# Optimization experiments

Measured on AMD Instinct MI355X. Metric: run time of the kernel, lower is better.

The kernel has to match this reference:

```python
import jax, jax.numpy as jnp
import numpy as np

B, S, HID = 4, 2048, 512
NH, HD = 8, 64
MAX_REL = 512


def setup_inputs() -> dict:
    key = jax.random.key(0)
    ks = jax.random.split(key, 10)
    sd = 0.02
    return {
        "hidden_states": jax.random.normal(ks[0], (B, S, HID), jnp.float32),
        "attention_mask": jnp.ones((B, S), jnp.float32),
        "Wq": jax.random.normal(ks[1], (HID, HID), jnp.float32) * sd,
        "bq": jnp.zeros((HID,), jnp.float32),
        "Wk": jax.random.normal(ks[2], (HID, HID), jnp.float32) * sd,
        "bk": jnp.zeros((HID,), jnp.float32),
        "Wv": jax.random.normal(ks[3], (HID, HID), jnp.float32) * sd,
        "bv": jnp.zeros((HID,), jnp.float32),
        "Wo": jax.random.normal(ks[4], (HID, HID), jnp.float32) * sd,
        "bo": jnp.zeros((HID,), jnp.float32),
        "rel_table": jax.random.normal(ks[5], (2 * MAX_REL + 1, NH), jnp.float32) * sd,
    }


def _heads(x):
    # [B,S,HID] -> [B,NH,S,HD]
    return x.reshape(B, S, NH, HD).transpose(0, 2, 1, 3)


def reference(hidden_states, attention_mask, Wq, bq, Wk, bk, Wv, bv, Wo, bo, rel_table):
    q = _heads(hidden_states @ Wq + bq)
    k = _heads(hidden_states @ Wk + bk)
    v = _heads(hidden_states @ Wv + bv)

    scores = jnp.einsum("bhqd,bhkd->bhqk", q, k) / jnp.sqrt(jnp.float32(HD))

    # relative position bias: rel[i,j] = clip(j-i, -MAX_REL, MAX_REL) + MAX_REL
    pos = jnp.arange(S)
    rel = jnp.clip(pos[None, :] - pos[:, None], -MAX_REL, MAX_REL) + MAX_REL
    bias = rel_table[rel]                      # [S,S,NH]
    bias = bias.transpose(2, 0, 1)             # [NH,S,S]
    scores = scores + bias[None]

    # mask: 1 attend, 0 masked
    neg = jnp.finfo(scores.dtype).min
    scores = scores + (1.0 - attention_mask)[:, None, None, :] * neg

    probs = jax.nn.softmax(scores, axis=-1)
    ctx = jnp.einsum("bhqk,bhkd->bhqd", probs, v)
    ctx = ctx.transpose(0, 2, 1, 3).reshape(B, S, HID)
    return ctx @ Wo + bo
```

## Files before the change

kernel.cpp:

```cpp
#include <hip/hip_runtime.h>
#include <hip/hip_bf16.h>

#define B_    4
#define S_    2048
#define HID_  512
#define NH_   8
#define HD_   64
#define MAXREL 512
#define M_    (B_ * S_)

#define LOG2E 1.44269504f
#define SCALE_Q (0.125f * LOG2E)

typedef __attribute__((ext_vector_type(8))) short bf8;
typedef __attribute__((ext_vector_type(4))) float f4;
typedef __attribute__((ext_vector_type(16))) float f16f;

static __device__ __forceinline__ unsigned short f2bf(float f) {
    union { float f; unsigned int u; } v; v.f = f;
    unsigned int u = v.u;
    unsigned int r = (u + 0x7FFFu + ((u >> 16) & 1u)) >> 16;
    return (unsigned short)r;
}

static __device__ __forceinline__ float ex2(float x) {
    float r; asm("v_exp_f32 %0, %1" : "=v"(r) : "v"(x)); return r;
}

static __device__ __forceinline__ void gload16(const void* g, void* l) {
    __builtin_amdgcn_global_load_lds(
        (const __attribute__((address_space(1))) unsigned int*)g,
        (__attribute__((address_space(3))) unsigned int*)l, 16, 0, 0);
}

#define MFMA16(a, b, c) __builtin_amdgcn_mfma_f32_16x16x32_bf16((a), (b), (c), 0, 0, 0)
#define MFMA32(a, b, c) __builtin_amdgcn_mfma_f32_32x32x16_bf16((a), (b), (c), 0, 0, 0)

__global__ void k_cast_hs(const float* __restrict__ src, unsigned short* __restrict__ dst, int n4) {
    int i = blockIdx.x * blockDim.x + threadIdx.x;
    if (i >= n4) return;
    float4 v = ((const float4*)src)[i];
    ushort4 o;
    o.x = f2bf(v.x); o.y = f2bf(v.y); o.z = f2bf(v.z); o.w = f2bf(v.w);
    ((ushort4*)dst)[i] = o;
}

__global__ void k_prep_mask(const float* __restrict__ mask, float* __restrict__ maskadd) {
    int i = blockIdx.x * blockDim.x + threadIdx.x;
    if (i < M_) maskadd[i] = (1.0f - mask[i]) * -3.0e38f;
}

__global__ void k_transpose_w4(const float* __restrict__ W0, const float* __restrict__ W1,
                               const float* __restrict__ W2, const float* __restrict__ W3,
                               unsigned short* __restrict__ T0, unsigned short* __restrict__ T1,
                               unsigned short* __restrict__ T2, unsigned short* __restrict__ T3) {
    __shared__ float tile[32][33];
    const int z = blockIdx.z;
    const float* W = (z == 0) ? W0 : (z == 1) ? W1 : (z == 2) ? W2 : W3;
    unsigned short* T = (z == 0) ? T0 : (z == 1) ? T1 : (z == 2) ? T2 : T3;
    const int tx = threadIdx.x & 31, ty = threadIdx.x >> 5;
    const int n0 = blockIdx.x * 32, k0 = blockIdx.y * 32;
    #pragma unroll
    for (int i = 0; i < 4; ++i)
        tile[ty + i * 8][tx] = W[(size_t)(k0 + ty + i * 8) * HID_ + n0 + tx];
    __syncthreads();
    #pragma unroll
    for (int i = 0; i < 4; ++i)
        T[(size_t)(n0 + ty + i * 8) * HID_ + k0 + tx] = f2bf(tile[tx][ty + i * 8]);
}

__global__ __launch_bounds__(256, 3) void k_gemm_qkv(
    const unsigned short* __restrict__ Abf,
    const unsigned short* __restrict__ Wqt, const unsigned short* __restrict__ Wkt,
    const unsigned short* __restrict__ Wvt,
    const float* __restrict__ bq, const float* __restrict__ bk, const float* __restrict__ bv,
    unsigned short* __restrict__ Q, unsigned short* __restrict__ K, unsigned short* __restrict__ Vt)
{
    __shared__ unsigned short Al[2][128 * 32];
    __shared__ unsigned short Bl[2][128 * 32];

    const int t = threadIdx.x;
    const int lane = t & 63, w = t >> 6;
    const int lr = lane & 15, lg = lane >> 4;
    const int wr = w >> 1, wc = w & 1;

    const int m0 = blockIdx.x * 128;
    const int ng = blockIdx.y * 128;
    const int z = ng >> 9;
    const int n0 = ng & 511;
    const unsigned short* Wt = (z == 0) ? Wqt : ((z == 1) ? Wkt : Wvt);
    const float* bias = (z == 0) ? bq : ((z == 1) ? bk : bv);
    const float osc = (z == 0) ? SCALE_Q : 1.0f;

    const int srow = t >> 2;
    const int sc = (((t & 3) ^ ((srow >> 1) & 3))) * 8;
    const unsigned short* Ag0 = &Abf[(size_t)(m0 + srow) * HID_ + sc];
    const unsigned short* Ag1 = &Abf[(size_t)(m0 + 64 + srow) * HID_ + sc];
    const unsigned short* Bg0 = &Wt[(size_t)(n0 + srow) * HID_ + sc];
    const unsigned short* Bg1 = &Wt[(size_t)(n0 + 64 + srow) * HID_ + sc];
    char* dA0 = (char*)&Al[0][0] + w * 1024;
    char* dB0 = (char*)&Bl[0][0] + w * 1024;

    const int fx = (lr >> 1) & 3;
    int aoff[4], boff[4];
    #pragma unroll
    for (int i = 0; i < 4; ++i) {
        aoff[i] = (wr * 64 + i * 16 + lr) * 32 + ((lg ^ fx) * 8);
        boff[i] = (wc * 64 + i * 16 + lr) * 32 + ((lg ^ fx) * 8);
    }

    gload16(Ag0, dA0);
    gload16(Ag1, dA0 + 4096);
    gload16(Bg0, dB0);
    gload16(Bg1, dB0 + 4096);
    __syncthreads();

    f4 acc[4][4] = {};
    for (int kt = 0; kt < 16; ++kt) {
        const int cur = kt & 1;
        if (kt < 15) {
            const int ko = (kt + 1) * 32;
            const int bo = (cur ^ 1) * 8192;
            gload16(Ag0 + ko, dA0 + bo);
            gload16(Ag1 + ko, dA0 + bo + 4096);
            gload16(Bg0 + ko, dB0 + bo);
            gload16(Bg1 + ko, dB0 + bo + 4096);
        }
        bf8 af[4], bf_[4];
        #pragma unroll
        for (int i = 0; i < 4; ++i) {
            af[i]  = *(const bf8*)&Al[cur][aoff[i]];
            bf_[i] = *(const bf8*)&Bl[cur][boff[i]];
        }
        #pragma unroll
        for (int mi = 0; mi < 4; ++mi)
            #pragma unroll
            for (int ni = 0; ni < 4; ++ni)
                acc[mi][ni] = MFMA16(af[mi], bf_[ni], acc[mi][ni]);
        __syncthreads();
    }

    #pragma unroll
    for (int mi = 0; mi < 4; ++mi)
    #pragma unroll
    for (int ni = 0; ni < 4; ++ni) {
        const int col = n0 + wc * 64 + ni * 16 + lr;
        const int h = col >> 6, d = col & 63;
        const float bs = bias[col];
        const int row0 = m0 + wr * 64 + mi * 16 + lg * 4;
        const int b = row0 >> 11, s0 = row0 & 2047;
        if (z == 2) {
            ushort4 o;
            o.x = f2bf(acc[mi][ni][0] + bs);
            o.y = f2bf(acc[mi][ni][1] + bs);
            o.z = f2bf(acc[mi][ni][2] + bs);
            o.w = f2bf(acc[mi][ni][3] + bs);
            *(ushort4*)&Vt[(((size_t)(b * NH_ + h)) * HD_ + d) * S_ + s0] = o;
        } else {
            unsigned short* dst = (z == 0) ? Q : K;
            #pragma unroll
            for (int r = 0; r < 4; ++r) {
                float v = (acc[mi][ni][r] + bs) * osc;
                dst[(((size_t)(b * NH_ + h)) * S_ + s0 + r) * HD_ + d] = f2bf(v);
            }
        }
    }
}

__global__ __launch_bounds__(512) void k_gemm_out(
    const unsigned short* __restrict__ Abf,
    const unsigned short* __restrict__ Wot,
    const float* __restrict__ bo,
    float* __restrict__ out)
{
    __shared__ unsigned short Al[2][128 * 32];
    __shared__ unsigned short Bl[2][128 * 32];

    const int t = threadIdx.x;
    const int lane = t & 63, w = t >> 6;
    const int lr = lane & 15, lg = lane >> 4;
    const int wr = w >> 2, wc = w & 3;

    const int m0 = blockIdx.x * 128;
    const int n0 = blockIdx.y * 128;

    const int srow = t >> 2;
    const int sc = (((t & 3) ^ ((srow >> 1) & 3))) * 8;
    const unsigned short* Ag = &Abf[(size_t)(m0 + srow) * HID_ + sc];
    const unsigned short* Bg = &Wot[(size_t)(n0 + srow) * HID_ + sc];
    char* dA = (char*)&Al[0][0] + w * 1024;
    char* dB = (char*)&Bl[0][0] + w * 1024;

    const int fx = (lr >> 1) & 3;
    int aoff[4], boff[2];
    #pragma unroll
    for (int i = 0; i < 4; ++i)
        aoff[i] = (wr * 64 + i * 16 + lr) * 32 + ((lg ^ fx) * 8);
    #pragma unroll
    for (int i = 0; i < 2; ++i)
        boff[i] = (wc * 32 + i * 16 + lr) * 32 + ((lg ^ fx) * 8);

    gload16(Ag, dA);
    gload16(Bg, dB);
    __syncthreads();

    f4 acc[4][2] = {};
    for (int kt = 0; kt < 16; ++kt) {
        const int cur = kt & 1;
        if (kt < 15) {
            const int ko = (kt + 1) * 32;
            const int bo_ = (cur ^ 1) * 8192;
            gload16(Ag + ko, dA + bo_);
            gload16(Bg + ko, dB + bo_);
        }
        bf8 af[4], bf_[2];
        #pragma unroll
        for (int i = 0; i < 4; ++i) af[i] = *(const bf8*)&Al[cur][aoff[i]];
        #pragma unroll
        for (int i = 0; i < 2; ++i) bf_[i] = *(const bf8*)&Bl[cur][boff[i]];
        #pragma unroll
        for (int mi = 0; mi < 4; ++mi)
            #pragma unroll
            for (int ni = 0; ni < 2; ++ni)
                acc[mi][ni] = MFMA16(af[mi], bf_[ni], acc[mi][ni]);
        __syncthreads();
    }

    #pragma unroll
    for (int mi = 0; mi < 4; ++mi)
    #pragma unroll
    for (int ni = 0; ni < 2; ++ni) {
        const int col = n0 + wc * 32 + ni * 16 + lr;
        const float bs = bo[col];
        const int row0 = m0 + wr * 64 + mi * 16 + lg * 4;
        #pragma unroll
        for (int r = 0; r < 4; ++r)
            out[(size_t)(row0 + r) * HID_ + col] = acc[mi][ni][r] + bs;
    }
}

__global__ __launch_bounds__(256, 2) void k_flash(
    const unsigned short* __restrict__ Q, const unsigned short* __restrict__ K,
    const unsigned short* __restrict__ Vt,
    const float* __restrict__ rel_table, const float* __restrict__ maskadd,
    unsigned short* __restrict__ ctx)
{
    __shared__ unsigned short Klds[2][4096];
    __shared__ unsigned short Vlds[2][4096];
    __shared__ unsigned short Ps[4][32][68];
    __shared__ float Tbp[2176];

    const int t = threadIdx.x;
    const int lane = t & 63, w = t >> 6;
    const int q = lane & 31, hi = lane >> 5;

    const int flat = blockIdx.x;
    const int idx = flat >> 3;
    const int bh = (flat & 7) * 4 + (idx >> 4);
    const int qb = idx & 15;
    const int b = bh >> 3, h = bh & 7;
    const int q0 = qb * 128;

    for (int i = t; i < 2176; i += 256) {
        int r = i - q0 - 127;
        r = r < -MAXREL ? -MAXREL : (r > MAXREL ? MAXREL : r);
        Tbp[i] = rel_table[(r + MAXREL) * NH_ + h] * LOG2E;
    }
    const float TbLo = rel_table[h] * LOG2E;
    const float TbHi = rel_table[2 * MAXREL * NH_ + h] * LOG2E;

    const unsigned short* Kb = K + (size_t)bh * S_ * HD_;
    const unsigned short* Vb = Vt + (size_t)bh * HD_ * S_;
    const float* mb = maskadd + b * S_;

    const int myq = q0 + w * 32 + q;
    const int qw = q0 + w * 32;
    bf8 qf[4];
    #pragma unroll
    for (int s = 0; s < 4; ++s)
        qf[s] = *(const bf8*)&Q[((size_t)bh * S_ + myq) * HD_ + s * 16 + hi * 8];

    const int srow = t >> 3, sslot = t & 7;
    const int sxor = (sslot ^ (srow & 7)) * 8;
    const size_t kb0 = (size_t)srow * HD_ + sxor;
    const size_t kb1 = (size_t)(srow + 32) * HD_ + sxor;
    const size_t vb0 = (size_t)srow * S_ + sxor;
    const size_t vb1 = (size_t)(srow + 32) * S_ + sxor;
    const int woff = w * 1024;

    f16f ca0 = {}, ca1 = {};
    float m_s = -INFINITY, lsum = 0.f;

    gload16(&Kb[kb0], (char*)&Klds[0][0] + woff);
    gload16(&Kb[kb1], (char*)&Klds[0][0] + 4096 + woff);
    gload16(&Vb[vb0], (char*)&Vlds[0][0] + woff);
    gload16(&Vb[vb1], (char*)&Vlds[0][0] + 4096 + woff);
    __syncthreads();

    const int xq = q & 7;
    const int jb0 = 127 - w * 32 - q + 4 * hi;
    for (int ti = 0; ti < 32; ++ti) {
        const int cur = ti & 1;
        const int kv0 = ti * 64;

        if (ti < 31) {
            const int nxt = cur ^ 1;
            const size_t ko = (size_t)(kv0 + 64) * HD_;
            gload16(&Kb[kb0 + ko], (char*)&Klds[nxt][0] + woff);
            gload16(&Kb[kb1 + ko], (char*)&Klds[nxt][0] + 4096 + woff);
            gload16(&Vb[vb0 + kv0 + 64], (char*)&Vlds[nxt][0] + woff);
            gload16(&Vb[vb1 + kv0 + 64], (char*)&Vlds[nxt][0] + 4096 + woff);
        }

        f16f sa0 = {}, sa1 = {};
        __builtin_amdgcn_s_setprio(1);
        #pragma unroll
        for (int s = 0; s < 4; ++s) {
            const int slot = ((2 * s + hi) ^ xq) * 8;
            bf8 k0 = *(const bf8*)&Klds[cur][q * 64 + slot];
            bf8 k1 = *(const bf8*)&Klds[cur][(q + 32) * 64 + slot];
            sa0 = MFMA32(k0, qf[s], sa0);
            sa1 = MFMA32(k1, qf[s], sa1);
        }
        __builtin_amdgcn_s_setprio(0);

        float tmaxl = -INFINITY;
        {
            const bool ulo = (kv0 + 31 - qw <= -MAXREL);
            const bool uhi = (kv0 - (qw + 31) >= MAXREL);
            if (ulo || uhi) {
                const float bc = ulo ? TbLo : TbHi;
                #pragma unroll
                for (int m = 0; m < 4; ++m) {
                    float4 mk = *(const float4*)&mb[kv0 + m * 8 + hi * 4];
                    #pragma unroll
                    for (int r = 0; r < 4; ++r) {
                        float mkv = (r == 0) ? mk.x : (r == 1) ? mk.y : (r == 2) ? mk.z : mk.w;
                        float sv = sa0[4 * m + r] + bc + mkv;
                        sa0[4 * m + r] = sv;
                        tmaxl = fmaxf(tmaxl, sv);
                    }
                }
            } else {
                #pragma unroll
                for (int m = 0; m < 4; ++m) {
                    float4 mk = *(const float4*)&mb[kv0 + m * 8 + hi * 4];
                    #pragma unroll
                    for (int r = 0; r < 4; ++r) {
                        float mkv = (r == 0) ? mk.x : (r == 1) ? mk.y : (r == 2) ? mk.z : mk.w;
                        float sv = sa0[4 * m + r] + Tbp[jb0 + kv0 + m * 8 + r] + mkv;
                        sa0[4 * m + r] = sv;
                        tmaxl = fmaxf(tmaxl, sv);
                    }
                }
            }
            const int kvh = kv0 + 32;
            const bool ulo1 = (kvh + 31 - qw <= -MAXREL);
            const bool uhi1 = (kvh - (qw + 31) >= MAXREL);
            if (ulo1 || uhi1) {
                const float bc = ulo1 ? TbLo : TbHi;
                #pragma unroll
                for (int m = 0; m < 4; ++m) {
                    float4 mk = *(const float4*)&mb[kvh + m * 8 + hi * 4];
                    #pragma unroll
                    for (int r = 0; r < 4; ++r) {
                        float mkv = (r == 0) ? mk.x : (r == 1) ? mk.y : (r == 2) ? mk.z : mk.w;
                        float sv = sa1[4 * m + r] + bc + mkv;
                        sa1[4 * m + r] = sv;
                        tmaxl = fmaxf(tmaxl, sv);
                    }
                }
            } else {
                #pragma unroll
                for (int m = 0; m < 4; ++m) {
                    float4 mk = *(const float4*)&mb[kvh + m * 8 + hi * 4];
                    #pragma unroll
                    for (int r = 0; r < 4; ++r) {
                        float mkv = (r == 0) ? mk.x : (r == 1) ? mk.y : (r == 2) ? mk.z : mk.w;
                        float sv = sa1[4 * m + r] + Tbp[jb0 + kvh + m * 8 + r] + mkv;
                        sa1[4 * m + r] = sv;
                        tmaxl = fmaxf(tmaxl, sv);
                    }
                }
            }
        }
        const float tmax = fmaxf(tmaxl, __shfl_xor(tmaxl, 32));

        float ptile = 0.f;
        unsigned int pkA[8], pkB[8];
        #pragma unroll
        for (int m = 0; m < 4; ++m) {
            float a0 = ex2(sa0[4 * m + 0] - m_s), a1 = ex2(sa0[4 * m + 1] - m_s);
            float a2 = ex2(sa0[4 * m + 2] - m_s), a3 = ex2(sa0[4 * m + 3] - m_s);
            float b0 = ex2(sa1[4 * m + 0] - m_s), b1 = ex2(sa1[4 * m + 1] - m_s);
            float b2 = ex2(sa1[4 * m + 2] - m_s), b3 = ex2(sa1[4 * m + 3] - m_s);
            ptile += ((a0 + a1) + (a2 + a3)) + ((b0 + b1) + (b2 + b3));
            asm("v_cvt_pk_bf16_f32 %0, %1, %2" : "=v"(pkA[2 * m])     : "v"(a0), "v"(a1));
            asm("v_cvt_pk_bf16_f32 %0, %1, %2" : "=v"(pkA[2 * m + 1]) : "v"(a2), "v"(a3));
            asm("v_cvt_pk_bf16_f32 %0, %1, %2" : "=v"(pkB[2 * m])     : "v"(b0), "v"(b1));
            asm("v_cvt_pk_bf16_f32 %0, %1, %2" : "=v"(pkB[2 * m + 1]) : "v"(b2), "v"(b3));
        }
        if (!__all(tmax <= m_s + 8.0f)) {
            const float mnew = fmaxf(m_s, tmax);
            const float fac = ex2(m_s - mnew);
            lsum *= fac;
            ca0 *= fac;
            ca1 *= fac;
            ptile = 0.f;
            #pragma unroll
            for (int m = 0; m < 4; ++m) {
                float a0 = ex2(sa0[4 * m + 0] - mnew), a1 = ex2(sa0[4 * m + 1] - mnew);
                float a2 = ex2(sa0[4 * m + 2] - mnew), a3 = ex2(sa0[4 * m + 3] - mnew);
                float b0 = ex2(sa1[4 * m + 0] - mnew), b1 = ex2(sa1[4 * m + 1] - mnew);
                float b2 = ex2(sa1[4 * m + 2] - mnew), b3 = ex2(sa1[4 * m + 3] - mnew);
                ptile += ((a0 + a1) + (a2 + a3)) + ((b0 + b1) + (b2 + b3));
                asm("v_cvt_pk_bf16_f32 %0, %1, %2" : "=v"(pkA[2 * m])     : "v"(a0), "v"(a1));
                asm("v_cvt_pk_bf16_f32 %0, %1, %2" : "=v"(pkA[2 * m + 1]) : "v"(a2), "v"(a3));
                asm("v_cvt_pk_bf16_f32 %0, %1, %2" : "=v"(pkB[2 * m])     : "v"(b0), "v"(b1));
                asm("v_cvt_pk_bf16_f32 %0, %1, %2" : "=v"(pkB[2 * m + 1]) : "v"(b2), "v"(b3));
            }
            m_s = mnew;
        }
        lsum += ptile;

        #pragma unroll
        for (int m = 0; m < 4; ++m) {
            uint2 pa; pa.x = pkA[2 * m]; pa.y = pkA[2 * m + 1];
            *(uint2*)&Ps[w][q][m * 8 + hi * 4] = pa;
            uint2 pb; pb.x = pkB[2 * m]; pb.y = pkB[2 * m + 1];
            *(uint2*)&Ps[w][q][32 + m * 8 + hi * 4] = pb;
        }
        asm volatile("s_waitcnt lgkmcnt(0)" ::: "memory");
        __builtin_amdgcn_sched_barrier(0);

        __builtin_amdgcn_s_setprio(1);
        #pragma unroll
        for (int s = 0; s < 4; ++s) {
            bf8 pf = *(const bf8*)&Ps[w][q][s * 16 + hi * 8];
            const int slot = ((2 * s + hi) ^ xq) * 8;
            bf8 v0 = *(const bf8*)&Vlds[cur][q * 64 + slot];
            bf8 v1 = *(const bf8*)&Vlds[cur][(q + 32) * 64 + slot];
            ca0 = MFMA32(v0, pf, ca0);
            ca1 = MFMA32(v1, pf, ca1);
        }
        __builtin_amdgcn_s_setprio(0);
        __syncthreads();
    }

    lsum += __shfl_xor(lsum, 32);
    const float inv = 1.0f / lsum;
    unsigned short* cg = &ctx[(size_t)(b * S_ + myq) * HID_ + h * HD_];
    #pragma unroll
    for (int m = 0; m < 4; ++m) {
        ushort4 o0;
        o0.x = f2bf(ca0[4 * m + 0] * inv);
        o0.y = f2bf(ca0[4 * m + 1] * inv);
        o0.z = f2bf(ca0[4 * m + 2] * inv);
        o0.w = f2bf(ca0[4 * m + 3] * inv);
        *(ushort4*)&cg[m * 8 + hi * 4] = o0;
        ushort4 o1;
        o1.x = f2bf(ca1[4 * m + 0] * inv);
        o1.y = f2bf(ca1[4 * m + 1] * inv);
        o1.z = f2bf(ca1[4 * m + 2] * inv);
        o1.w = f2bf(ca1[4 * m + 3] * inv);
        *(ushort4*)&cg[32 + m * 8 + hi * 4] = o1;
    }
}

extern "C" void kernel_launch(void* const* d_in, const int* in_sizes, int n_in,
                              void* d_out, int out_size, void* d_ws, size_t ws_size,
                              hipStream_t stream) {
    const float* hs  = (const float*)d_in[0];
    const float* msk = (const float*)d_in[1];
    const float* Wq  = (const float*)d_in[2];
    const float* bq  = (const float*)d_in[3];
    const float* Wk  = (const float*)d_in[4];
    const float* bk  = (const float*)d_in[5];
    const float* Wv  = (const float*)d_in[6];
    const float* bv  = (const float*)d_in[7];
    const float* Wo  = (const float*)d_in[8];
    const float* bo  = (const float*)d_in[9];
    const float* rel = (const float*)d_in[10];
    float* out = (float*)d_out;

    char* ws = (char*)d_ws;
    unsigned short* hsb = (unsigned short*)ws; ws += (size_t)M_ * HID_ * 2;
    unsigned short* Wqt = (unsigned short*)ws; ws += (size_t)HID_ * HID_ * 2;
    unsigned short* Wkt = (unsigned short*)ws; ws += (size_t)HID_ * HID_ * 2;
    unsigned short* Wvt = (unsigned short*)ws; ws += (size_t)HID_ * HID_ * 2;
    unsigned short* Wot = (unsigned short*)ws; ws += (size_t)HID_ * HID_ * 2;
    unsigned short* Qb  = (unsigned short*)ws; ws += (size_t)M_ * HID_ * 2;
    unsigned short* Kb  = (unsigned short*)ws; ws += (size_t)M_ * HID_ * 2;
    unsigned short* Vtb = (unsigned short*)ws; ws += (size_t)M_ * HID_ * 2;
    unsigned short* ctxb= (unsigned short*)ws; ws += (size_t)M_ * HID_ * 2;
    float* maskadd      = (float*)ws;          ws += (size_t)M_ * 4;

    k_cast_hs<<<(M_ * HID_ / 4 + 255) / 256, 256, 0, stream>>>(hs, hsb, M_ * HID_ / 4);
    k_prep_mask<<<(M_ + 255) / 256, 256, 0, stream>>>(msk, maskadd);
    k_transpose_w4<<<dim3(16, 16, 4), 256, 0, stream>>>(Wq, Wk, Wv, Wo, Wqt, Wkt, Wvt, Wot);
    k_gemm_qkv<<<dim3(64, 12), 256, 0, stream>>>(
        hsb, Wqt, Wkt, Wvt, bq, bk, bv, Qb, Kb, Vtb);
    k_flash<<<512, 256, 0, stream>>>(Qb, Kb, Vtb, rel, maskadd, ctxb);
    k_gemm_out<<<dim3(64, 4), 512, 0, stream>>>(ctxb, Wot, bo, out);
}
```

Baseline: 119.8 us.

## Triple-buffer K/V loads, pass P via permlane swap, cache mask in LDS

```diff
diff --git a/kernel.cpp b/kernel.cpp
--- a/kernel.cpp
+++ b/kernel.cpp
@@ -31,6 +31,11 @@
     __builtin_amdgcn_global_load_lds(
         (const __attribute__((address_space(1))) unsigned int*)g,
         (__attribute__((address_space(3))) unsigned int*)l, 16, 0, 0);
+}
+
+static __device__ __forceinline__ bf8 mkbf8(unsigned a, unsigned b, unsigned c, unsigned d) {
+    uint4 u = make_uint4(a, b, c, d);
+    return *(bf8*)&u;
 }
 
 #define MFMA16(a, b, c) __builtin_amdgcn_mfma_f32_16x16x32_bf16((a), (b), (c), 0, 0, 0)
@@ -245,10 +250,9 @@
     const float* __restrict__ rel_table, const float* __restrict__ maskadd,
     unsigned short* __restrict__ ctx)
 {
-    __shared__ unsigned short Klds[2][4096];
-    __shared__ unsigned short Vlds[2][4096];
-    __shared__ unsigned short Ps[4][32][68];
+    __shared__ unsigned short KV[3][8192];
     __shared__ float Tbp[2176];
+    __shared__ float maskc[S_];
 
     const int t = threadIdx.x;
     const int lane = t & 63, w = t >> 6;
@@ -266,12 +270,16 @@
         r = r < -MAXREL ? -MAXREL : (r > MAXREL ? MAXREL : r);
         Tbp[i] = rel_table[(r + MAXREL) * NH_ + h] * LOG2E;
     }
+    {
+        const float4* src = (const float4*)(maskadd + b * S_);
+        float4* dst = (float4*)maskc;
+        for (int i = t; i < S_ / 4; i += 256) dst[i] = src[i];
+    }
     const float TbLo = rel_table[h] * LOG2E;
     const float TbHi = rel_table[2 * MAXREL * NH_ + h] * LOG2E;
 
     const unsigned short* Kb = K + (size_t)bh * S_ * HD_;
     const unsigned short* Vb = Vt + (size_t)bh * HD_ * S_;
-    const float* mb = maskadd + b * S_;
 
     const int myq = q0 + w * 32 + q;
     const int qw = q0 + w * 32;
@@ -288,37 +296,46 @@
     const size_t vb1 = (size_t)(srow + 32) * S_ + sxor;
     const int woff = w * 1024;
 
+    auto stage = [&](int kvt, int buf) {
+        char* base = (char*)&KV[buf][0];
+        const size_t ko = (size_t)kvt * 64 * HD_;
+        const size_t vo = (size_t)kvt * 64;
+        gload16(&Kb[kb0 + ko], base + woff);
+        gload16(&Kb[kb1 + ko], base + 4096 + woff);
+        gload16(&Vb[vb0 + vo], base + 8192 + woff);
+        gload16(&Vb[vb1 + vo], base + 8192 + 4096 + woff);
+    };
+
     f16f ca0 = {}, ca1 = {};
     float m_s = -INFINITY, lsum = 0.f;
 
-    gload16(&Kb[kb0], (char*)&Klds[0][0] + woff);
-    gload16(&Kb[kb1], (char*)&Klds[0][0] + 4096 + woff);
-    gload16(&Vb[vb0], (char*)&Vlds[0][0] + woff);
-    gload16(&Vb[vb1], (char*)&Vlds[0][0] + 4096 + woff);
-    __syncthreads();
+    stage(0, 0);
+    stage(1, 1);
+    asm volatile("s_waitcnt lgkmcnt(0)" ::: "memory");
+    asm volatile("s_waitcnt vmcnt(4)" ::: "memory");
+    __builtin_amdgcn_s_barrier();
+    __builtin_amdgcn_sched_barrier(0);
 
     const int xq = q & 7;
     const int jb0 = 127 - w * 32 - q + 4 * hi;
+    int cur = 0;
     for (int ti = 0; ti < 32; ++ti) {
-        const int cur = ti & 1;
         const int kv0 = ti * 64;
 
-        if (ti < 31) {
-            const int nxt = cur ^ 1;
-            const size_t ko = (size_t)(kv0 + 64) * HD_;
-            gload16(&Kb[kb0 + ko], (char*)&Klds[nxt][0] + woff);
-            gload16(&Kb[kb1 + ko], (char*)&Klds[nxt][0] + 4096 + woff);
-            gload16(&Vb[vb0 + kv0 + 64], (char*)&Vlds[nxt][0] + woff);
-            gload16(&Vb[vb1 + kv0 + 64], (char*)&Vlds[nxt][0] + 4096 + woff);
-        }
+        if (ti < 30) {
+            int nb = cur + 2; if (nb >= 3) nb -= 3;
+            stage(ti + 2, nb);
+        }
+        const unsigned short* Kt  = &KV[cur][0];
+        const unsigned short* Vtl = &KV[cur][4096];
 
         f16f sa0 = {}, sa1 = {};
         __builtin_amdgcn_s_setprio(1);
         #pragma unroll
         for (int s = 0; s < 4; ++s) {
             const int slot = ((2 * s + hi) ^ xq) * 8;
-            bf8 k0 = *(const bf8*)&Klds[cur][q * 64 + slot];
-            bf8 k1 = *(const bf8*)&Klds[cur][(q + 32) * 64 + slot];
+            bf8 k0 = *(const bf8*)&Kt[q * 64 + slot];
+            bf8 k1 = *(const bf8*)&Kt[(q + 32) * 64 + slot];
             sa0 = MFMA32(k0, qf[s], sa0);
             sa1 = MFMA32(k1, qf[s], sa1);
         }
@@ -332,7 +349,7 @@
                 const float bc = ulo ? TbLo : TbHi;
                 #pragma unroll
                 for (int m = 0; m < 4; ++m) {
-                    float4 mk = *(const float4*)&mb[kv0 + m * 8 + hi * 4];
+                    float4 mk = *(const float4*)&maskc[kv0 + m * 8 + hi * 4];
                     #pragma unroll
                     for (int r = 0; r < 4; ++r) {
                         float mkv = (r == 0) ? mk.x : (r == 1) ? mk.y : (r == 2) ? mk.z : mk.w;
@@ -344,7 +361,7 @@
             } else {
                 #pragma unroll
                 for (int m = 0; m < 4; ++m) {
-                    float4 mk = *(const float4*)&mb[kv0 + m * 8 + hi * 4];
+                    float4 mk = *(const float4*)&maskc[kv0 + m * 8 + hi * 4];
                     #pragma unroll
                     for (int r = 0; r < 4; ++r) {
                         float mkv = (r == 0) ? mk.x : (r == 1) ? mk.y : (r == 2) ? mk.z : mk.w;
@@ -361,7 +378,7 @@
                 const float bc = ulo1 ? TbLo : TbHi;
                 #pragma unroll
                 for (int m = 0; m < 4; ++m) {
-                    float4 mk = *(const float4*)&mb[kvh + m * 8 + hi * 4];
+                    float4 mk = *(const float4*)&maskc[kvh + m * 8 + hi * 4];
                     #pragma unroll
                     for (int r = 0; r < 4; ++r) {
                         float mkv = (r == 0) ? mk.x : (r == 1) ? mk.y : (r == 2) ? mk.z : mk.w;
@@ -373,7 +390,7 @@
             } else {
                 #pragma unroll
                 for (int m = 0; m < 4; ++m) {
-                    float4 mk = *(const float4*)&mb[kvh + m * 8 + hi * 4];
+                    float4 mk = *(const float4*)&maskc[kvh + m * 8 + hi * 4];
                     #pragma unroll
                     for (int r = 0; r < 4; ++r) {
                         float mkv = (r == 0) ? mk.x : (r == 1) ? mk.y : (r == 2) ? mk.z : mk.w;
@@ -423,28 +440,42 @@
         }
         lsum += ptile;
 
-        #pragma unroll
-        for (int m = 0; m < 4; ++m) {
-            uint2 pa; pa.x = pkA[2 * m]; pa.y = pkA[2 * m + 1];
-            *(uint2*)&Ps[w][q][m * 8 + hi * 4] = pa;
-            uint2 pb; pb.x = pkB[2 * m]; pb.y = pkB[2 * m + 1];
-            *(uint2*)&Ps[w][q][32 + m * 8 + hi * 4] = pb;
-        }
-        asm volatile("s_waitcnt lgkmcnt(0)" ::: "memory");
-        __builtin_amdgcn_sched_barrier(0);
+        bf8 pf[4];
+        #pragma unroll
+        for (int s2 = 0; s2 < 2; ++s2) {
+            unsigned c0 = pkA[4 * s2],     c2 = pkA[4 * s2 + 2];
+            unsigned c1 = pkA[4 * s2 + 1], c3 = pkA[4 * s2 + 3];
+            asm("v_permlane32_swap_b32 %0, %1" : "+v"(c0), "+v"(c2));
+            asm("v_permlane32_swap_b32 %0, %1" : "+v"(c1), "+v"(c3));
+            pf[s2] = mkbf8(c0, c1, c2, c3);
+        }
+        #pragma unroll
+        for (int s2 = 0; s2 < 2; ++s2) {
+            unsigned c0 = pkB[4 * s2],     c2 = pkB[4 * s2 + 2];
+            unsigned c1 = pkB[4 * s2 + 1], c3 = pkB[4 * s2 + 3];
+            asm("v_permlane32_swap_b32 %0, %1" : "+v"(c0), "+v"(c2));
+            asm("v_permlane32_swap_b32 %0, %1" : "+v"(c1), "+v"(c3));
+            pf[2 + s2] = mkbf8(c0, c1, c2, c3);
+        }
 
         __builtin_amdgcn_s_setprio(1);
         #pragma unroll
         for (int s = 0; s < 4; ++s) {
-            bf8 pf = *(const bf8*)&Ps[w][q][s * 16 + hi * 8];
             const int slot = ((2 * s + hi) ^ xq) * 8;
-            bf8 v0 = *(const bf8*)&Vlds[cur][q * 64 + slot];
-            bf8 v1 = *(const bf8*)&Vlds[cur][(q + 32) * 64 + slot];
-            ca0 = MFMA32(v0, pf, ca0);
-            ca1 = MFMA32(v1, pf, ca1);
+            bf8 v0 = *(const bf8*)&Vtl[q * 64 + slot];
+            bf8 v1 = *(const bf8*)&Vtl[(q + 32) * 64 + slot];
+            ca0 = MFMA32(v0, pf[s], ca0);
+            ca1 = MFMA32(v1, pf[s], ca1);
         }
         __builtin_amdgcn_s_setprio(0);
-        __syncthreads();
+
+        if (ti < 31) {
+            if (ti < 30) asm volatile("s_waitcnt vmcnt(4)" ::: "memory");
+            else         asm volatile("s_waitcnt vmcnt(0)" ::: "memory");
+            __builtin_amdgcn_s_barrier();
+            __builtin_amdgcn_sched_barrier(0);
+        }
+        cur = (cur == 2) ? 0 : cur + 1;
     }
 
     lsum += __shfl_xor(lsum, 32);
```

New measurement: 111.8 us. 1.07x faster.
